# Performance work log

Hardware: AMD Instinct MI355X
Metric: run time of the kernel (lower is better)

Reference implementation:

```python
import jax, jax.numpy as jnp
import numpy as np

H_D, W_D = 64, 64          # 1024x1024 image / 16 patch size
N = H_D * W_D              # 4096 patches
D = 768                    # DINO ViT-B/16 embed dim
ALPHA = 0.5
K = 100


def setup_inputs() -> dict:
    key = jax.random.key(0)
    k1, k2 = jax.random.split(key)
    out = jax.random.normal(k1, (N, D), dtype=jnp.float32)
    attn_seed = jax.random.randint(k2, (2,), 0, H_D, dtype=jnp.int32)
    return {"out": out, "attn_seed": attn_seed}


def _connected_components(mask):
    """8-connectivity connected components via iterative min-label propagation.
    Background = 0. Foreground pixels get the minimum initial id (+1) of their
    component (same partition as cv2.connectedComponents, different numbering)."""
    fg = mask > 0
    BIG = jnp.int32(N + 1)
    init = jnp.where(fg, jnp.arange(N, dtype=jnp.int32).reshape(H_D, W_D) + 1, BIG)

    def step(l):
        p = jnp.pad(l, 1, constant_values=N + 1)
        m = l
        for dy in (0, 1, 2):          # fixed 3x3 neighborhood, not a data-dim loop
            for dx in (0, 1, 2):
                m = jnp.minimum(m, p[dy:dy + H_D, dx:dx + W_D])
        return jnp.where(fg, m, BIG)

    def cond(st):
        l, prev = st
        return jnp.any(l != prev)

    def body(st):
        l, _ = st
        return step(l), l

    l, _ = jax.lax.while_loop(cond, body, (step(init), init))
    return jnp.where(fg, l, 0)


def reference(out, attn_seed):
    # similarity between all patch features: [N, N]
    sim = out @ out.T
    deg = sim >= 0                                        # degree_matrix (bool)
    # patch with fewest non-negative similarities
    seed_degree_flat = jnp.argmin(deg.sum(axis=0)).astype(jnp.int32)
    seed_degree = jnp.stack([seed_degree_flat // W_D, seed_degree_flat % W_D])
    # blend degree seed with attention seed
    seed_rc = jnp.round(ALPHA * seed_degree + (1.0 - ALPHA) * attn_seed).astype(jnp.int32)
    seed = seed_rc[0] * W_D + seed_rc[1]

    # initial expansion set = patches positively correlated with the seed
    s = deg[seed].astype(jnp.int32)
    s = s.at[seed].set(1)                                 # degree_matrix[seed][seed] = 255 (truthy)
    order = jnp.argsort(-sim[seed])                       # descending
    s = s.at[order[K:]].set(0)                            # keep top-k most similar

    # sequential seed expansion (updates feed into later iterations)
    def step(s, i):
        grows = jnp.sum(sim[i] * (s == 1)) > 0
        s = s.at[i].set(jnp.where(s[i] == 0, 0, jnp.where(grows, 1, 0)))
        return s, None

    s, _ = jax.lax.scan(step, s, jnp.arange(N))

    return _connected_components(s.reshape(H_D, W_D))
```

## Files before the change

kernel.cpp:

```cpp
#include <hip/hip_runtime.h>
#include <cstdint>

#define NP   4096
#define DD   768
#define HD   64
#define WD   64
#define KTOP 100
#define BIGL 4097

typedef short bf16x8 __attribute__((ext_vector_type(8)));
typedef float f32x4  __attribute__((ext_vector_type(4)));

__device__ __forceinline__ void gload_lds16(const void* g, void* l) {
    __builtin_amdgcn_global_load_lds(
        (const __attribute__((address_space(1))) unsigned int*)(uintptr_t)g,
        (__attribute__((address_space(3))) unsigned int*)(unsigned int)(uintptr_t)l,
        16, 0, 0);
}

__device__ __forceinline__ unsigned short f2bf_rne(float x) {
    unsigned b = __float_as_uint(x);
    unsigned r = b + 0x7FFFu + ((b >> 16) & 1u);
    return (unsigned short)(r >> 16);
}
__device__ __forceinline__ float bf2f(unsigned short h) {
    return __uint_as_float(((unsigned)h) << 16);
}

__global__ __launch_bounds__(256) void k_split(const float* __restrict__ A,
                                               unsigned short* __restrict__ hi,
                                               unsigned short* __restrict__ lo,
                                               int* __restrict__ counts) {
    if (blockIdx.x < 16) counts[blockIdx.x * 256 + threadIdx.x] = 0;
    int idx = blockIdx.x * 256 + threadIdx.x;
    float4 v = ((const float4*)A)[idx];
    unsigned short h0 = f2bf_rne(v.x), h1 = f2bf_rne(v.y),
                   h2 = f2bf_rne(v.z), h3 = f2bf_rne(v.w);
    unsigned short l0 = f2bf_rne(v.x - bf2f(h0)), l1 = f2bf_rne(v.y - bf2f(h1)),
                   l2 = f2bf_rne(v.z - bf2f(h2)), l3 = f2bf_rne(v.w - bf2f(h3));
    ((ushort4*)hi)[idx] = make_ushort4(h0, h1, h2, h3);
    ((ushort4*)lo)[idx] = make_ushort4(l0, l1, l2, l3);
}

__device__ __forceinline__ void stage_group(const unsigned short* __restrict__ hi,
                                            const unsigned short* __restrict__ lo,
                                            int i0, int j0, int kbase, int tid,
                                            unsigned short* G) {
#pragma unroll
    for (int q = 0; q < 8; ++q) {
        int pp = q * 256 + tid;
        int ppt = pp & 1023;
        int row = ppt >> 3;
        int kcl = (ppt & 7) ^ (row & 7);
        int rbase = (pp < 1024) ? i0 : j0;
        const unsigned short* src =
            ((kcl < 4) ? hi : lo) + (size_t)(rbase + row) * DD + kbase + (kcl & 3) * 8;
        gload_lds16(src, G + pp * 8);
    }
}

__global__ __launch_bounds__(256, 2) void k_gemm(const unsigned short* __restrict__ hi,
                                                 const unsigned short* __restrict__ lo,
                                                 int* __restrict__ counts) {
    __shared__ __align__(16) unsigned short G[2][2048 * 8];
    __shared__ int colc[128];
    __shared__ int rowc[128];

    int t = ((blockIdx.x & 7) * 66) + (blockIdx.x >> 3);
    int SI = 0, SJ = 0, rem = t;
    for (;;) {
        int sz = (SI == SJ) ? 36 : 64;
        if (rem < sz) break;
        rem -= sz;
        if (++SJ == 4) { ++SI; SJ = SI; }
    }
    int li, lj;
    if (SI == SJ) {
        int r = 0;
        while (rem >= (8 - r)) { rem -= (8 - r); ++r; }
        li = r; lj = r + rem;
    } else { li = rem >> 3; lj = rem & 7; }
    int bi = SI * 8 + li, bj = SJ * 8 + lj;
    int i0 = bi * 128, j0 = bj * 128;

    int tid = threadIdx.x;
    int lane = tid & 63, w = tid >> 6;
    int wm = w & 1, wn = w >> 1;

    f32x4 acc[4][4];
#pragma unroll
    for (int ti = 0; ti < 4; ++ti)
#pragma unroll
        for (int u = 0; u < 4; ++u) { acc[ti][u][0] = 0.f; acc[ti][u][1] = 0.f;
                                      acc[ti][u][2] = 0.f; acc[ti][u][3] = 0.f; }

    int kcf = lane >> 4;
    int paH[4], paL[4], pbH[4], pbL[4];
#pragma unroll
    for (int tt = 0; tt < 4; ++tt) {
        int arow = wm * 64 + tt * 16 + (lane & 15);
        paH[tt] = arow * 8 + (kcf ^ (arow & 7));
        paL[tt] = arow * 8 + ((kcf + 4) ^ (arow & 7));
    }
#pragma unroll
    for (int u = 0; u < 4; ++u) {
        int brow = wn * 64 + u * 16 + (lane & 15);
        pbH[u] = 1024 + brow * 8 + (kcf ^ (brow & 7));
        pbL[u] = 1024 + brow * 8 + ((kcf + 4) ^ (brow & 7));
    }

    stage_group(hi, lo, i0, j0, 0, tid, G[0]);
    for (int it = 0; it < 24; ++it) {
        int cur = it & 1;
        if (it < 23) {
            stage_group(hi, lo, i0, j0, (it + 1) * 32, tid, G[cur ^ 1]);
            asm volatile("s_waitcnt vmcnt(8)" ::: "memory");
        } else {
            asm volatile("s_waitcnt vmcnt(0)" ::: "memory");
        }
        __builtin_amdgcn_s_barrier();

        bf16x8 ahi[4], alo[4], bhi[4], blo[4];
#pragma unroll
        for (int tt = 0; tt < 4; ++tt) {
            ahi[tt] = *(const bf16x8*)&G[cur][paH[tt] * 8];
            alo[tt] = *(const bf16x8*)&G[cur][paL[tt] * 8];
        }
#pragma unroll
        for (int u = 0; u < 4; ++u) {
            bhi[u] = *(const bf16x8*)&G[cur][pbH[u] * 8];
            blo[u] = *(const bf16x8*)&G[cur][pbL[u] * 8];
        }
        asm volatile("s_waitcnt lgkmcnt(0)" ::: "memory");
        __builtin_amdgcn_s_barrier();

        __builtin_amdgcn_s_setprio(1);
#pragma unroll
        for (int ti = 0; ti < 4; ++ti)
#pragma unroll
            for (int u = 0; u < 4; ++u) {
                acc[ti][u] = __builtin_amdgcn_mfma_f32_16x16x32_bf16(
                    ahi[ti], bhi[u], acc[ti][u], 0, 0, 0);
                acc[ti][u] = __builtin_amdgcn_mfma_f32_16x16x32_bf16(
                    alo[ti], bhi[u], acc[ti][u], 0, 0, 0);
                acc[ti][u] = __builtin_amdgcn_mfma_f32_16x16x32_bf16(
                    ahi[ti], blo[u], acc[ti][u], 0, 0, 0);
            }
        __builtin_amdgcn_s_setprio(0);
    }

    if (tid < 128) { colc[tid] = 0; rowc[tid] = 0; }
    __syncthreads();

    int nl = lane & 15;
    int rg = lane >> 4;
#pragma unroll
    for (int u = 0; u < 4; ++u) {
        int v = 0;
#pragma unroll
        for (int ti = 0; ti < 4; ++ti) {
            f32x4 a = acc[ti][u];
            v += ((a[0] >= 0.f) ? 1 : 0) + ((a[1] >= 0.f) ? 1 : 0) +
                 ((a[2] >= 0.f) ? 1 : 0) + ((a[3] >= 0.f) ? 1 : 0);
        }
        v += __shfl_xor(v, 16);
        v += __shfl_xor(v, 32);
        if (rg == 0) atomicAdd(&colc[wn * 64 + u * 16 + nl], v);
    }
    if (bi != bj) {
#pragma unroll
        for (int ti = 0; ti < 4; ++ti)
#pragma unroll
            for (int g = 0; g < 4; ++g) {
                int rv = ((acc[ti][0][g] >= 0.f) ? 1 : 0) +
                         ((acc[ti][1][g] >= 0.f) ? 1 : 0) +
                         ((acc[ti][2][g] >= 0.f) ? 1 : 0) +
                         ((acc[ti][3][g] >= 0.f) ? 1 : 0);
                rv += __shfl_xor(rv, 1);
                rv += __shfl_xor(rv, 2);
                rv += __shfl_xor(rv, 4);
                rv += __shfl_xor(rv, 8);
                if (nl == 0) atomicAdd(&rowc[wm * 64 + ti * 16 + rg * 4 + g], rv);
            }
    }
    __syncthreads();
    if (tid < 128) {
        atomicAdd(&counts[j0 + tid], colc[tid]);
        if (bi != bj) atomicAdd(&counts[i0 + tid], rowc[tid]);
    }
}

__device__ __forceinline__ int block_sum256(int v, int lane, int w, int* wred) {
#pragma unroll
    for (int o = 1; o < 64; o <<= 1) v += __shfl_xor(v, o);
    if (lane == 0) wred[w] = v;
    __syncthreads();
    int tt = wred[0] + wred[1] + wred[2] + wred[3];
    __syncthreads();
    return tt;
}
__device__ __forceinline__ int block_exscan256(int v, int lane, int w, int* wred,
                                               int* total) {
    int inc = v;
#pragma unroll
    for (int o = 1; o < 64; o <<= 1) { int u = __shfl_up(inc, o); if (lane >= o) inc += u; }
    if (lane == 63) wred[w] = inc;
    __syncthreads();
    int w0 = wred[0], w1 = wred[1], w2 = wred[2], w3 = wred[3];
    int wofs = (w > 0 ? w0 : 0) + (w > 1 ? w1 : 0) + (w > 2 ? w2 : 0);
    *total = w0 + w1 + w2 + w3;
    __syncthreads();
    return wofs + inc - v;
}

__global__ __launch_bounds__(256) void k_seedrow(const float* __restrict__ A,
                                                 const int* __restrict__ counts,
                                                 const int* __restrict__ attn_seed,
                                                 float* __restrict__ simrow,
                                                 int* __restrict__ seedp,
                                                 int* __restrict__ outp) {
    __shared__ int redA[256], redB[256];
    int tid = threadIdx.x, lane = tid & 63, w = tid >> 6;
    int blk = blockIdx.x;

    int bc = 0x7fffffff, bI = 0;
    for (int j = tid; j < NP; j += 256) {
        int c = counts[j];
        if (c < bc) { bc = c; bI = j; }
    }
    redA[tid] = bc; redB[tid] = bI;
    __syncthreads();
    for (int st = 128; st > 0; st >>= 1) {
        if (tid < st) {
            if (redA[tid + st] < redA[tid] ||
                (redA[tid + st] == redA[tid] && redB[tid + st] < redB[tid])) {
                redA[tid] = redA[tid + st];
                redB[tid] = redB[tid + st];
            }
        }
        __syncthreads();
    }
    int flat = redB[0];
    int sr = flat / WD, sc = flat % WD;
    int vr = sr + attn_seed[0];
    int vc = sc + attn_seed[1];
    int rr, rc;
    if ((vr & 1) == 0) rr = vr >> 1;
    else { int m = vr >> 1; rr = (m & 1) ? m + 1 : m; }
    if ((vc & 1) == 0) rc = vc >> 1;
    else { int m = vc >> 1; rc = (m & 1) ? m + 1 : m; }
    int seed = rr * WD + rc;
    if (blk == 0 && tid == 0) seedp[0] = seed;

    float sv[12];
#pragma unroll
    for (int kk = 0; kk < 12; ++kk) sv[kk] = A[(size_t)seed * DD + lane + kk * 64];
    int jbase = blk * 32 + w * 8;
    for (int jj = 0; jj < 8; ++jj) {
        int j = jbase + jj;
        float sum = 0.f;
#pragma unroll
        for (int kk = 0; kk < 12; ++kk)
            sum += sv[kk] * A[(size_t)j * DD + lane + kk * 64];
#pragma unroll
        for (int o = 32; o > 0; o >>= 1) sum += __shfl_down(sum, o);
        if (lane == 0) simrow[j] = sum;
    }
    if (tid < 32) outp[blk * 32 + tid] = 0;
}

__global__ __launch_bounds__(256) void k_sel(const float* __restrict__ simrow,
                                             const int* __restrict__ seedp,
                                             int* __restrict__ act, int* __restrict__ Mp) {
    __shared__ int wred[4];
    int tid = threadIdx.x, lane = tid & 63, w = tid >> 6;
    int seed = seedp[0];
    int base = tid * 16;
    unsigned key[16];
#pragma unroll
    for (int n = 0; n < 16; ++n) {
        unsigned b = __float_as_uint(simrow[base + n]);
        key[n] = (b & 0x80000000u) ? ~b : (b | 0x80000000u);
    }
    unsigned prefix = 0;
    for (int bit = 31; bit >= 0; --bit) {
        unsigned cand = prefix | (1u << bit);
        int c = 0;
#pragma unroll
        for (int n = 0; n < 16; ++n) c += (key[n] >= cand) ? 1 : 0;
        int tot = block_sum256(c, lane, w, wred);
        if (tot >= KTOP) prefix = cand;
    }
    unsigned KT = prefix;
    int cgt = 0, ceq = 0;
#pragma unroll
    for (int n = 0; n < 16; ++n) {
        cgt += (key[n] > KT) ? 1 : 0;
        ceq += (key[n] == KT) ? 1 : 0;
    }
    int totgt = block_sum256(cgt, lane, w, wred);
    int slots = KTOP - totgt;
    int dummy;
    int eqrun = block_exscan256(ceq, lane, w, wred, &dummy);
    int flag[16]; int cf = 0;
#pragma unroll
    for (int n = 0; n < 16; ++n) {
        int j = base + n;
        unsigned k = key[n];
        int topk = (k > KT) || (k == KT && eqrun < slots);
        if (k == KT) ++eqrun;
        int f = (topk && (k >= 0x80000000u || j == seed)) ? 1 : 0;
        flag[n] = f; cf += f;
    }
    int M;
    int off = block_exscan256(cf, lane, w, wred, &M);
    if (tid == 0) Mp[0] = M;
#pragma unroll
    for (int n = 0; n < 16; ++n)
        if (flag[n]) act[off++] = base + n;
}

__global__ __launch_bounds__(256) void k_sub(const float* __restrict__ A,
                                             const int* __restrict__ act,
                                             const int* __restrict__ Mp,
                                             float* __restrict__ subsim) {
    __shared__ float av[DD];
    int M = Mp[0];
    int p = blockIdx.x;
    if (p >= M) return;
    int tid = threadIdx.x, lane = tid & 63, w = tid >> 6;
    int ip = act[p];
    for (int k = tid; k < DD; k += 256) av[k] = A[(size_t)ip * DD + k];
    __syncthreads();
    for (int q = w; q < M; q += 4) {
        int iq = act[q];
        float sum = 0.f;
#pragma unroll
        for (int kk = 0; kk < 12; ++kk) {
            int k = lane + kk * 64;
            sum += av[k] * A[(size_t)iq * DD + k];
        }
#pragma unroll
        for (int o = 32; o > 0; o >>= 1) sum += __shfl_down(sum, o);
        if (lane == 0) subsim[p * 128 + q] = sum;
    }
}

__global__ __launch_bounds__(256) void k_fin(const float* __restrict__ subsim,
                                             const int* __restrict__ act,
                                             const int* __restrict__ Mp,
                                             int* __restrict__ outp) {
    __shared__ float ss[128 * 128];
    __shared__ int act_s[128];
    __shared__ int alive[128];
    __shared__ int lab[128];
    __shared__ unsigned char nbr[128][8];
    __shared__ int ncnt[128];
    __shared__ int chg;
    int M = Mp[0];
    int tid = threadIdx.x, lane = tid & 63;

    if (tid < 128) act_s[tid] = (tid < 128 && tid < M) ? act[tid] : 0;
    for (int i4 = tid; i4 < M * 32; i4 += 256) {
        int p = i4 >> 5, qb = (i4 & 31) << 2;
        float4 v = ((const float4*)subsim)[i4];
        ss[(qb + 0) * 128 + ((p + qb + 0) & 127)] = v.x;
        ss[(qb + 1) * 128 + ((p + qb + 1) & 127)] = v.y;
        ss[(qb + 2) * 128 + ((p + qb + 2) & 127)] = v.z;
        ss[(qb + 3) * 128 + ((p + qb + 3) & 127)] = v.w;
    }
    __syncthreads();

    if (tid < 64) {
        float S_lo = 0.f, S_hi = 0.f;
        for (int q = 0; q < M; ++q) {
            S_lo += ss[q * 128 + ((lane + q) & 127)];
            S_hi += ss[q * 128 + ((lane + 64 + q) & 127)];
        }
        float al = (lane < M) ? 1.f : 0.f;
        float ah = (lane + 64 < M) ? 1.f : 0.f;
        for (int p = 0; p < M; ++p) {
            float Sp = (p < 64) ? __shfl(S_lo, p) : __shfl(S_hi, p - 64);
            if (!(Sp > 0.f)) {
                S_lo -= ss[p * 128 + ((lane + p) & 127)];
                S_hi -= ss[p * 128 + ((lane + 64 + p) & 127)];
                if (lane == p)      al = 0.f;
                if (lane + 64 == p) ah = 0.f;
            }
        }
        alive[lane]      = (lane < M && al != 0.f) ? 1 : 0;
        alive[lane + 64] = (lane + 64 < M && ah != 0.f) ? 1 : 0;
    }
    __syncthreads();

    if (tid < 128) {
        int a = (tid < M) ? alive[tid] : 0;
        int c = 0;
        if (a) {
            int id = act_s[tid];
            int y = id >> 6, x = id & 63;
            for (int q = 0; q < M; ++q) {
                if (q == tid || !alive[q]) continue;
                int qid = act_s[q];
                int dy = (qid >> 6) - y, dx = (qid & 63) - x;
                if (dy >= -1 && dy <= 1 && dx >= -1 && dx <= 1)
                    nbr[tid][c++] = (unsigned char)q;
            }
        }
        ncnt[tid] = c;
        lab[tid] = a ? tid : 32767;
    }
    __syncthreads();
    while (true) {
        if (tid == 0) chg = 0;
        __syncthreads();
        int local = 0;
        if (tid < M && alive[tid]) {
            int m = lab[tid];
            int nc = ncnt[tid];
            for (int k = 0; k < nc; ++k) { int u = lab[nbr[tid][k]]; if (u < m) m = u; }
            { int u = lab[m]; if (u < m) m = u; }
            { int u = lab[m]; if (u < m) m = u; }
            if (m < lab[tid]) { lab[tid] = m; local = 1; }
        }
        if (local) chg = 1;
        __syncthreads();
        if (chg == 0) break;
        __syncthreads();
    }
    if (tid < M && alive[tid]) outp[act_s[tid]] = act_s[lab[tid]] + 1;
}

extern "C" void kernel_launch(void* const* d_in, const int* in_sizes, int n_in,
                              void* d_out, int out_size, void* d_ws, size_t ws_size,
                              hipStream_t stream) {
    const float* A = (const float*)d_in[0];
    const int* attn = (const int*)d_in[1];
    int* outp = (int*)d_out;

    char* ws = (char*)d_ws;
    int*            counts = (int*)(ws);
    float*          simrow = (float*)(ws + 16384);
    int*            act    = (int*)(ws + 32768);
    int*            Mp     = (int*)(ws + 33280);
    int*            seedp  = (int*)(ws + 33284);
    float*          subsim = (float*)(ws + 33792);
    unsigned short* hi     = (unsigned short*)(ws + 1048576);
    unsigned short* lo     = (unsigned short*)(ws + 1048576 + 6291456);

    k_split  <<<3072, 256, 0, stream>>>(A, hi, lo, counts);
    k_gemm   <<<528,  256, 0, stream>>>(hi, lo, counts);
    k_seedrow<<<128,  256, 0, stream>>>(A, counts, attn, simrow, seedp, outp);
    k_sel    <<<1,    256, 0, stream>>>(simrow, seedp, act, Mp);
    k_sub    <<<128,  256, 0, stream>>>(A, act, Mp, subsim);
    k_fin    <<<1,    256, 0, stream>>>(subsim, act, Mp, outp);
}
```

Baseline: 193.8 us.

## Single-buffer GEMM LDS for higher occupancy and fuse top-k select into subsim kernel

The GEMM drops from double-buffered to single-buffered LDS and reuses that buffer for the epilogue counters. Launch bounds rise to 4 blocks per CU, trading in-block prefetch overlap for more resident waves to hide latency. Separately, the single-block top-k selection kernel is merged into the subsimilarity kernel: every block redundantly recomputes the selection and block 0 writes the shared results, removing one launch and its serialization.

```diff
diff --git a/kernel.cpp b/kernel.cpp
--- a/kernel.cpp
+++ b/kernel.cpp
@@ -59,12 +59,10 @@
     }
 }
 
-__global__ __launch_bounds__(256, 2) void k_gemm(const unsigned short* __restrict__ hi,
+__global__ __launch_bounds__(256, 4) void k_gemm(const unsigned short* __restrict__ hi,
                                                  const unsigned short* __restrict__ lo,
                                                  int* __restrict__ counts) {
-    __shared__ __align__(16) unsigned short G[2][2048 * 8];
-    __shared__ int colc[128];
-    __shared__ int rowc[128];
+    __shared__ __align__(16) unsigned short G[2048 * 8];
 
     int t = ((blockIdx.x & 7) * 66) + (blockIdx.x >> 3);
     int SI = 0, SJ = 0, rem = t;
@@ -109,30 +107,28 @@
         pbL[u] = 1024 + brow * 8 + ((kcf + 4) ^ (brow & 7));
     }
 
-    stage_group(hi, lo, i0, j0, 0, tid, G[0]);
+    stage_group(hi, lo, i0, j0, 0, tid, G);
     for (int it = 0; it < 24; ++it) {
-        int cur = it & 1;
-        if (it < 23) {
-            stage_group(hi, lo, i0, j0, (it + 1) * 32, tid, G[cur ^ 1]);
-            asm volatile("s_waitcnt vmcnt(8)" ::: "memory");
-        } else {
-            asm volatile("s_waitcnt vmcnt(0)" ::: "memory");
-        }
+        asm volatile("s_waitcnt vmcnt(0)" ::: "memory");
         __builtin_amdgcn_s_barrier();
 
         bf16x8 ahi[4], alo[4], bhi[4], blo[4];
 #pragma unroll
         for (int tt = 0; tt < 4; ++tt) {
-            ahi[tt] = *(const bf16x8*)&G[cur][paH[tt] * 8];
-            alo[tt] = *(const bf16x8*)&G[cur][paL[tt] * 8];
+            ahi[tt] = *(const bf16x8*)&G[paH[tt] * 8];
+            alo[tt] = *(const bf16x8*)&G[paL[tt] * 8];
         }
 #pragma unroll
         for (int u = 0; u < 4; ++u) {
-            bhi[u] = *(const bf16x8*)&G[cur][pbH[u] * 8];
-            blo[u] = *(const bf16x8*)&G[cur][pbL[u] * 8];
+            bhi[u] = *(const bf16x8*)&G[pbH[u] * 8];
+            blo[u] = *(const bf16x8*)&G[pbL[u] * 8];
         }
         asm volatile("s_waitcnt lgkmcnt(0)" ::: "memory");
+        __builtin_amdgcn_sched_barrier(0);
         __builtin_amdgcn_s_barrier();
+
+        if (it + 1 < 24)
+            stage_group(hi, lo, i0, j0, (it + 1) * 32, tid, G);
 
         __builtin_amdgcn_s_setprio(1);
 #pragma unroll
@@ -149,6 +145,9 @@
         __builtin_amdgcn_s_setprio(0);
     }
 
+    __syncthreads();
+    int* colc = (int*)G;
+    int* rowc = ((int*)G) + 128;
     if (tid < 128) { colc[tid] = 0; rowc[tid] = 0; }
     __syncthreads();
 
@@ -269,10 +268,14 @@
     if (tid < 32) outp[blk * 32 + tid] = 0;
 }
 
-__global__ __launch_bounds__(256) void k_sel(const float* __restrict__ simrow,
-                                             const int* __restrict__ seedp,
-                                             int* __restrict__ act, int* __restrict__ Mp) {
+__global__ __launch_bounds__(256) void k_subsel(const float* __restrict__ A,
+                                                const float* __restrict__ simrow,
+                                                const int* __restrict__ seedp,
+                                                int* __restrict__ act, int* __restrict__ Mp,
+                                                float* __restrict__ subsim) {
     __shared__ int wred[4];
+    __shared__ int act_s[128];
+    __shared__ float av[DD];
     int tid = threadIdx.x, lane = tid & 63, w = tid >> 6;
     int seed = seedp[0];
     int base = tid * 16;
@@ -314,26 +317,23 @@
     }
     int M;
     int off = block_exscan256(cf, lane, w, wred, &M);
-    if (tid == 0) Mp[0] = M;
 #pragma unroll
     for (int n = 0; n < 16; ++n)
-        if (flag[n]) act[off++] = base + n;
-}
-
-__global__ __launch_bounds__(256) void k_sub(const float* __restrict__ A,
-                                             const int* __restrict__ act,
-                                             const int* __restrict__ Mp,
-                                             float* __restrict__ subsim) {
-    __shared__ float av[DD];
-    int M = Mp[0];
+        if (flag[n]) act_s[off++] = base + n;
+    __syncthreads();
+
     int p = blockIdx.x;
+    if (p == 0) {
+        if (tid == 0) Mp[0] = M;
+        if (tid < M) act[tid] = act_s[tid];
+    }
     if (p >= M) return;
-    int tid = threadIdx.x, lane = tid & 63, w = tid >> 6;
-    int ip = act[p];
+
+    int ip = act_s[p];
     for (int k = tid; k < DD; k += 256) av[k] = A[(size_t)ip * DD + k];
     __syncthreads();
     for (int q = w; q < M; q += 4) {
-        int iq = act[q];
+        int iq = act_s[q];
         float sum = 0.f;
 #pragma unroll
         for (int kk = 0; kk < 12; ++kk) {
@@ -360,7 +360,7 @@
     int M = Mp[0];
     int tid = threadIdx.x, lane = tid & 63;
 
-    if (tid < 128) act_s[tid] = (tid < 128 && tid < M) ? act[tid] : 0;
+    if (tid < 128) act_s[tid] = (tid < M) ? act[tid] : 0;
     for (int i4 = tid; i4 < M * 32; i4 += 256) {
         int p = i4 >> 5, qb = (i4 & 31) << 2;
         float4 v = ((const float4*)subsim)[i4];
@@ -451,7 +451,6 @@
     k_split  <<<3072, 256, 0, stream>>>(A, hi, lo, counts);
     k_gemm   <<<528,  256, 0, stream>>>(hi, lo, counts);
     k_seedrow<<<128,  256, 0, stream>>>(A, counts, attn, simrow, seedp, outp);
-    k_sel    <<<1,    256, 0, stream>>>(simrow, seedp, act, Mp);
-    k_sub    <<<128,  256, 0, stream>>>(A, act, Mp, subsim);
+    k_subsel <<<128,  256, 0, stream>>>(A, simrow, seedp, act, Mp, subsim);
     k_fin    <<<1,    256, 0, stream>>>(subsim, act, Mp, outp);
 }
```

New measurement: 332.3 us. 71.4% more time.
